# Kernel tuning notes

Measured on AMD Instinct MI355X. Metric: run time of the kernel, lower is better.

## Reference

```python
import jax, jax.numpy as jnp
import numpy as np

HEAD_SIZE = 64
N_EMBD = 768

def setup_inputs() -> dict:
    key = jax.random.key(0)
    kx, kq, kk, kv = jax.random.split(key, 4)
    x = jax.random.normal(kx, (4, 4096, N_EMBD), dtype=jnp.float32)
    s = 1.0 / np.sqrt(N_EMBD)
    Wq = jax.random.normal(kq, (N_EMBD, HEAD_SIZE), dtype=jnp.float32) * s
    Wk = jax.random.normal(kk, (N_EMBD, HEAD_SIZE), dtype=jnp.float32) * s
    Wv = jax.random.normal(kv, (N_EMBD, HEAD_SIZE), dtype=jnp.float32) * s
    return {"x": x, "Wq": Wq, "Wk": Wk, "Wv": Wv}

def reference(x, Wq, Wk, Wv):
    b, t, c = x.shape
    h = Wq.shape[1]
    q = jnp.einsum('btc,ch->bth', x, Wq)
    k = jnp.einsum('btc,ch->bth', x, Wk)
    v = jnp.einsum('btc,ch->bth', x, Wv)
    scores = jnp.einsum('bqh,bkh->bqk', q, k) / jnp.sqrt(jnp.float32(h))
    causal = jnp.tril(jnp.ones((t, t), dtype=bool))  # [t,t]
    scores = jnp.where(causal, scores, -jnp.inf)
    attn = jax.nn.softmax(scores, axis=-1)
    return jnp.einsum('bqk,bkh->bqh', attn, v)
```

## Files before the change

### kernel.cpp

```cpp
#include <hip/hip_runtime.h>
#include <math.h>

#define BB 4
#define TT 4096
#define CC 768
#define HH 64
#define NN 192
#define LDP 72
#define GR 32
#define XSTR 776
#define SC2 0.180336880f

typedef __bf16 bf16x8 __attribute__((ext_vector_type(8)));
typedef float floatx4 __attribute__((ext_vector_type(4)));
typedef float floatx16 __attribute__((ext_vector_type(16)));
typedef unsigned short u16x8 __attribute__((ext_vector_type(8)));

__device__ inline unsigned short f2bf(float f) {
    union { __bf16 b; unsigned short u; } v;
    v.b = (__bf16)f;
    return v.u;
}
__device__ inline float bf2f(unsigned short u) {
    union { unsigned int u; float f; } v;
    v.u = (unsigned int)u << 16;
    return v.f;
}
__device__ inline unsigned cvtpk(float lo, float hi) {
    unsigned d;
    asm("v_cvt_pk_bf16_f32 %0, %1, %2" : "=v"(d) : "v"(lo), "v"(hi));
    return d;
}

__global__ __launch_bounds__(256) void wprep(const float* __restrict__ Wq,
                                             const float* __restrict__ Wk,
                                             const float* __restrict__ Wv,
                                             unsigned short* __restrict__ wtf) {
    const int idx = blockIdx.x * 256 + threadIdx.x;
    if (idx >= NN * CC) return;
    const int j = idx & 7;
    const int lane = (idx >> 3) & 63;
    const int rest = idx >> 9;
    const int kg = rest % 24;
    const int n_tile = rest / 24;
    const int c = kg * 32 + (lane >> 4) * 8 + j;
    const int n = n_tile * 16 + (lane & 15);
    const float* W = (n < 64) ? Wq : (n < 128) ? Wk : Wv;
    wtf[idx] = f2bf(W[c * HH + (n & 63)]);
}

__global__ __launch_bounds__(256) void qkv_gemm(const float* __restrict__ x,
                                                const unsigned short* __restrict__ wtf,
                                                unsigned short* __restrict__ qb,
                                                unsigned short* __restrict__ kb,
                                                unsigned short* __restrict__ vbt) {
    __shared__ unsigned short As[GR * XSTR];

    const int tid = threadIdx.x;
    const int w = tid >> 6, lane = tid & 63;
    const int l15 = lane & 15, quad = lane >> 4;
    const int m0 = blockIdx.x * GR;
    const int n0 = w * 48;
    const int nt0 = w * 3;

    const float* xbase = x + (size_t)m0 * CC;
#pragma unroll
    for (int e = 0; e < 12; ++e) {
        const int c = tid + 256 * e;
        const int r = c / 96, off = (c - r * 96) * 8;
        const float4 v0 = *(const float4*)(xbase + (size_t)c * 8);
        const float4 v1 = *(const float4*)(xbase + (size_t)c * 8 + 4);
        u16x8 pk;
        pk[0] = f2bf(v0.x); pk[1] = f2bf(v0.y); pk[2] = f2bf(v0.z); pk[3] = f2bf(v0.w);
        pk[4] = f2bf(v1.x); pk[5] = f2bf(v1.y); pk[6] = f2bf(v1.z); pk[7] = f2bf(v1.w);
        *(u16x8*)(As + r * XSTR + off) = pk;
    }
    __syncthreads();

    floatx4 acc[2][3] = {};
#pragma unroll 4
    for (int step = 0; step < 12; ++step) {
        bf16x8 a0[2], a1[2];
#pragma unroll
        for (int rg = 0; rg < 2; ++rg) {
            const unsigned short* ap = As + (16 * rg + l15) * XSTR + step * 64 + quad * 8;
            a0[rg] = *(const bf16x8*)(ap);
            a1[rg] = *(const bf16x8*)(ap + 32);
        }
#pragma unroll
        for (int j = 0; j < 3; ++j) {
            const unsigned short* bp =
                wtf + ((size_t)((nt0 + j) * 24 + 2 * step) * 64 + lane) * 8;
            const bf16x8 b0 = *(const bf16x8*)(bp);
            const bf16x8 b1 = *(const bf16x8*)(bp + 512);
#pragma unroll
            for (int rg = 0; rg < 2; ++rg) {
                acc[rg][j] = __builtin_amdgcn_mfma_f32_16x16x32_bf16(a0[rg], b0, acc[rg][j], 0, 0, 0);
                acc[rg][j] = __builtin_amdgcn_mfma_f32_16x16x32_bf16(a1[rg], b1, acc[rg][j], 0, 0, 0);
            }
        }
    }

    const int b = m0 >> 12;
#pragma unroll
    for (int j = 0; j < 3; ++j) {
        const int n = n0 + j * 16 + l15;
        const int mid = n >> 6;
        const int h = n & 63;
#pragma unroll
        for (int rg = 0; rg < 2; ++rg) {
            const int tloc = (m0 & (TT - 1)) + 16 * rg + quad * 4;
            if (mid == 2) {
                ushort4 pk;
                pk.x = f2bf(acc[rg][j][0]); pk.y = f2bf(acc[rg][j][1]);
                pk.z = f2bf(acc[rg][j][2]); pk.w = f2bf(acc[rg][j][3]);
                *(ushort4*)(vbt + ((size_t)b * HH + h) * TT + tloc) = pk;
            } else {
                unsigned short* dst = (mid == 0) ? qb : kb;
#pragma unroll
                for (int r = 0; r < 4; ++r)
                    dst[(size_t)(m0 + 16 * rg + quad * 4 + r) * HH + h] = f2bf(acc[rg][j][r]);
            }
        }
    }
}

template<int CH>
__global__ __launch_bounds__(256) void attn_part(const unsigned short* __restrict__ qb,
                                                 const unsigned short* __restrict__ kb,
                                                 const unsigned short* __restrict__ vbt,
                                                 unsigned short* __restrict__ Opart,
                                                 float* __restrict__ lsum,
                                                 float* __restrict__ out) {
    __shared__ float Osh[2][2][16][64];
    __shared__ float Lsh[2][64];

    constexpr int NG = 64 / CH;
    constexpr int TOTB = CH * (NG * (NG + 1)) / 2;

    const int b = blockIdx.x & 3;
    int rem = TOTB - 1 - (blockIdx.x >> 2);
    int g = 0;
    while (rem >= CH * (g + 1)) { rem -= CH * (g + 1); ++g; }
    const int qt = g * CH + rem / (g + 1);
    const int ch = rem - (rem / (g + 1)) * (g + 1);

    const int q0  = qt * 64;
    const int tid = threadIdx.x;
    const int w = tid >> 6, lane = tid & 63;
    const int wq = w >> 1, wk = w & 1;
    const int l31 = lane & 31, hi = lane >> 5;

    const unsigned short* Qb  = qb  + (size_t)b * TT * HH;
    const unsigned short* Kb  = kb  + (size_t)b * TT * HH;
    const unsigned short* VTb = vbt + (size_t)b * HH * TT;

    bf16x8 qf[4];
    {
        const unsigned short* qp = Qb + (size_t)(q0 + 32 * wq + l31) * HH + 8 * hi;
#pragma unroll
        for (int s = 0; s < 4; ++s) qf[s] = *(const bf16x8*)(qp + 16 * s);
    }

    floatx16 o0 = {}, o1 = {};
    float lacc = 0.f;

    const int kt0 = ch * CH;
    const int kt1 = min(kt0 + CH, qt + 1);

    const unsigned short* kbase = Kb + (size_t)(32 * wk + l31) * HH + 8 * hi;
    bf16x8 kn[4];
#pragma unroll
    for (int s = 0; s < 4; ++s)
        kn[s] = *(const bf16x8*)(kbase + (size_t)kt0 * 64 * HH + 16 * s);

    for (int kt = kt0; kt < kt1; ++kt) {
        bf16x8 kc[4];
#pragma unroll
        for (int s = 0; s < 4; ++s) kc[s] = kn[s];

        bf16x8 vv[4];
#pragma unroll
        for (int i = 0; i < 4; ++i) {
            const int db = i >> 1, m = i & 1;
            vv[i] = *(const bf16x8*)(VTb + (size_t)(32 * db + l31) * TT
                                     + kt * 64 + 32 * wk + 16 * m + 8 * hi);
        }
        if (kt + 1 < kt1) {
#pragma unroll
            for (int s = 0; s < 4; ++s)
                kn[s] = *(const bf16x8*)(kbase + (size_t)(kt + 1) * 64 * HH + 16 * s);
        }

        floatx16 sa = {};
#pragma unroll
        for (int s = 0; s < 4; ++s)
            sa = __builtin_amdgcn_mfma_f32_32x32x16_bf16(kc[s], qf[s], sa, 0, 0, 0);

        float st[16];
#pragma unroll
        for (int r = 0; r < 16; ++r) st[r] = sa[r] * SC2;

        if (kt == qt) {
            const int qloc = 32 * wq + l31;
#pragma unroll
            for (int r = 0; r < 16; ++r) {
                const int kloc = 32 * wk + (r & 3) + 8 * (r >> 2) + 4 * hi;
                if (kloc > qloc) st[r] = -INFINITY;
            }
        }

#pragma unroll
        for (int r = 0; r < 16; ++r) {
            const float p = exp2f(st[r]);
            st[r] = p;
            lacc += p;
        }

        bf16x8 pf[2];
#pragma unroll
        for (int m = 0; m < 2; ++m) {
            const unsigned d0 = cvtpk(st[8 * m + 0], st[8 * m + 1]);
            const unsigned d1 = cvtpk(st[8 * m + 2], st[8 * m + 3]);
            const unsigned d2 = cvtpk(st[8 * m + 4], st[8 * m + 5]);
            const unsigned d3 = cvtpk(st[8 * m + 6], st[8 * m + 7]);
            const unsigned e0 = (unsigned)__shfl_xor((int)d0, 32);
            const unsigned e1 = (unsigned)__shfl_xor((int)d1, 32);
            const unsigned e2 = (unsigned)__shfl_xor((int)d2, 32);
            const unsigned e3 = (unsigned)__shfl_xor((int)d3, 32);
            union { unsigned u[4]; bf16x8 v; } pk;
            pk.u[0] = hi ? e2 : d0;
            pk.u[1] = hi ? e3 : d1;
            pk.u[2] = hi ? d2 : e0;
            pk.u[3] = hi ? d3 : e1;
            pf[m] = pk.v;
        }

        o0 = __builtin_amdgcn_mfma_f32_32x32x16_bf16(vv[0], pf[0], o0, 0, 0, 0);
        o0 = __builtin_amdgcn_mfma_f32_32x32x16_bf16(vv[1], pf[1], o0, 0, 0, 0);
        o1 = __builtin_amdgcn_mfma_f32_32x32x16_bf16(vv[2], pf[0], o1, 0, 0, 0);
        o1 = __builtin_amdgcn_mfma_f32_32x32x16_bf16(vv[3], pf[1], o1, 0, 0, 0);
    }

    if (wk == 1) {
#pragma unroll
        for (int r = 0; r < 16; ++r) {
            Osh[wq][0][r][lane] = o0[r];
            Osh[wq][1][r][lane] = o1[r];
        }
        Lsh[wq][lane] = lacc;
    }
    __syncthreads();
    if (wk == 1) return;
#pragma unroll
    for (int r = 0; r < 16; ++r) {
        o0[r] += Osh[wq][0][r][lane];
        o1[r] += Osh[wq][1][r][lane];
    }
    lacc += Lsh[wq][lane];
    const float l = lacc + __shfl_xor(lacc, 32);

    if (qt < CH) {
        float* outp = out + ((size_t)b * TT + q0 + 32 * wq + l31) * HH;
        const float inv = 1.f / l;
#pragma unroll
        for (int r = 0; r < 16; ++r) {
            const int dd = (r & 3) + 8 * (r >> 2) + 4 * hi;
            outp[dd]      = o0[r] * inv;
            outp[32 + dd] = o1[r] * inv;
        }
        return;
    }

    const int pbase = ((b * 64 + qt) * NG + ch) * 64;
    unsigned short* Op = Opart + ((size_t)pbase + 32 * wq + l31) * HH;
#pragma unroll
    for (int a = 0; a < 4; ++a) {
        *(unsigned*)(Op + 8 * a + 4 * hi)          = cvtpk(o0[4 * a + 0], o0[4 * a + 1]);
        *(unsigned*)(Op + 8 * a + 4 * hi + 2)      = cvtpk(o0[4 * a + 2], o0[4 * a + 3]);
        *(unsigned*)(Op + 32 + 8 * a + 4 * hi)     = cvtpk(o1[4 * a + 0], o1[4 * a + 1]);
        *(unsigned*)(Op + 32 + 8 * a + 4 * hi + 2) = cvtpk(o1[4 * a + 2], o1[4 * a + 3]);
    }
    if (hi == 0) lsum[pbase + 32 * wq + l31] = l;
}

template<int CH>
__global__ __launch_bounds__(256) void attn_merge(const unsigned short* __restrict__ Opart,
                                                  const float* __restrict__ lsum,
                                                  float* __restrict__ out) {
    constexpr int NG = 64 / CH;
    const int g = blockIdx.x * 256 + threadIdx.x;
    const int row = g >> 3, oct = g & 7;
    const int b = row >> 12, t = row & (TT - 1);
    const int qt = t >> 6, rloc = t & 63;
    if (qt < CH) return;
    const int nchunk = qt / CH + 1;
    const int pbase = ((b * 64 + qt) * NG) * 64 + rloc;
    const int d0 = oct * 8;

    float L = 0.f;
    float a[8] = {};
    for (int c = 0; c < nchunk; ++c) {
        const int idx = pbase + c * 64;
        L += lsum[idx];
        const u16x8 pv = *(const u16x8*)(Opart + (size_t)idx * HH + d0);
#pragma unroll
        for (int k = 0; k < 8; ++k) a[k] += bf2f(pv[k]);
    }
    const float inv = 1.f / L;
    float4 o0, o1;
    o0.x = a[0] * inv; o0.y = a[1] * inv; o0.z = a[2] * inv; o0.w = a[3] * inv;
    o1.x = a[4] * inv; o1.y = a[5] * inv; o1.z = a[6] * inv; o1.w = a[7] * inv;
    float* dst = out + (size_t)row * HH + d0;
    *(float4*)(dst) = o0;
    *(float4*)(dst + 4) = o1;
}

__global__ __launch_bounds__(256) void attn_full(const unsigned short* __restrict__ qb,
                                                 const unsigned short* __restrict__ kb,
                                                 const unsigned short* __restrict__ vbt,
                                                 float* __restrict__ out) {
    __shared__ unsigned short Ks[64 * LDP];
    __shared__ unsigned short VTs[64 * LDP];
    __shared__ unsigned short Ps[4][16 * LDP];

    const int b   = blockIdx.x >> 6;
    const int qt  = blockIdx.x & 63;
    const int q0  = qt * 64;
    const int tid = threadIdx.x;
    const int w = tid >> 6, lane = tid & 63;
    const int l15 = lane & 15, quad = lane >> 4;

    const unsigned short* Qb  = qb  + (size_t)b * TT * HH;
    const unsigned short* Kb  = kb  + (size_t)b * TT * HH;
    const unsigned short* VTb = vbt + (size_t)b * HH * TT;

    const int qrow = q0 + 16 * w + l15;
    const bf16x8 qf0 = *(const bf16x8*)(Qb + (size_t)qrow * HH + quad * 8);
    const bf16x8 qf1 = *(const bf16x8*)(Qb + (size_t)qrow * HH + 32 + quad * 8);

    floatx4 O[4] = {};
    floatx4 lacc = {0.f, 0.f, 0.f, 0.f};

    for (int kt = 0; kt <= qt; ++kt) {
        __syncthreads();
        const unsigned short* Kt = Kb + (size_t)(kt * 64) * HH;
        const unsigned short* Vt = VTb + kt * 64;
#pragma unroll
        for (int e = 0; e < 2; ++e) {
            const int chunk = tid + 256 * e;
            const int r = chunk >> 3, c0 = (chunk & 7) * 8;
            *(u16x8*)(Ks + r * LDP + c0)  = *(const u16x8*)(Kt + r * HH + c0);
            *(u16x8*)(VTs + r * LDP + c0) = *(const u16x8*)(Vt + (size_t)r * TT + c0);
        }
        __syncthreads();

        floatx4 s[4];
#pragma unroll
        for (int ki = 0; ki < 4; ++ki) {
            const bf16x8 kf0 = *(const bf16x8*)(Ks + (16 * ki + l15) * LDP + quad * 8);
            const bf16x8 kf1 = *(const bf16x8*)(Ks + (16 * ki + l15) * LDP + 32 + quad * 8);
            floatx4 c = {};
            c = __builtin_amdgcn_mfma_f32_16x16x32_bf16(qf0, kf0, c, 0, 0, 0);
            c = __builtin_amdgcn_mfma_f32_16x16x32_bf16(qf1, kf1, c, 0, 0, 0);
            s[ki] = c * SC2;
        }
        if (kt == qt) {
#pragma unroll
            for (int ki = 0; ki < 4; ++ki)
#pragma unroll
                for (int r = 0; r < 4; ++r)
                    if (16 * ki + l15 > 16 * w + quad * 4 + r) s[ki][r] = -INFINITY;
        }
#pragma unroll
        for (int ki = 0; ki < 4; ++ki)
#pragma unroll
            for (int r = 0; r < 4; ++r) {
                const float p = exp2f(s[ki][r]);
                s[ki][r] = p; lacc[r] += p;
            }

        unsigned short* Pw = Ps[w];
#pragma unroll
        for (int ki = 0; ki < 4; ++ki)
#pragma unroll
            for (int r = 0; r < 4; ++r)
                Pw[(quad * 4 + r) * LDP + 16 * ki + l15] = f2bf(s[ki][r]);

        const bf16x8 pf0 = *(const bf16x8*)(Pw + l15 * LDP + quad * 8);
        const bf16x8 pf1 = *(const bf16x8*)(Pw + l15 * LDP + 32 + quad * 8);
#pragma unroll
        for (int di = 0; di < 4; ++di) {
            const bf16x8 vf0 = *(const bf16x8*)(VTs + (16 * di + l15) * LDP + quad * 8);
            const bf16x8 vf1 = *(const bf16x8*)(VTs + (16 * di + l15) * LDP + 32 + quad * 8);
            O[di] = __builtin_amdgcn_mfma_f32_16x16x32_bf16(pf0, vf0, O[di], 0, 0, 0);
            O[di] = __builtin_amdgcn_mfma_f32_16x16x32_bf16(pf1, vf1, O[di], 0, 0, 0);
        }
    }
    float l_r[4];
#pragma unroll
    for (int r = 0; r < 4; ++r) {
        float v = lacc[r];
#pragma unroll
        for (int msk = 8; msk >= 1; msk >>= 1) v += __shfl_xor(v, msk, 64);
        l_r[r] = v;
    }
    float* outp = out + ((size_t)b * TT + q0 + 16 * w) * HH;
#pragma unroll
    for (int di = 0; di < 4; ++di)
#pragma unroll
        for (int r = 0; r < 4; ++r)
            outp[(quad * 4 + r) * HH + 16 * di + l15] = O[di][r] / l_r[r];
}

extern "C" void kernel_launch(void* const* d_in, const int* in_sizes, int n_in,
                              void* d_out, int out_size, void* d_ws, size_t ws_size,
                              hipStream_t stream) {
    const float* x  = (const float*)d_in[0];
    const float* Wq = (const float*)d_in[1];
    const float* Wk = (const float*)d_in[2];
    const float* Wv = (const float*)d_in[3];
    float* out = (float*)d_out;

    const size_t nQKV = (size_t)BB * TT * HH;
    unsigned short* qb  = (unsigned short*)d_ws;
    unsigned short* kb  = qb + nQKV;
    unsigned short* vbt = kb + nQKV;
    unsigned short* wtf = vbt + nQKV;
    unsigned short* Opart = wtf + (size_t)NN * CC;

    const size_t prows8  = (size_t)BB * 64 * 8 * 64;
    const size_t prows16 = (size_t)BB * 64 * 4 * 64;
    float* lsum8  = (float*)(Opart + prows8 * HH);
    float* lsum16 = (float*)(Opart + prows16 * HH);
    const size_t need8  = (size_t)((char*)(lsum8  + prows8)  - (char*)d_ws);
    const size_t need16 = (size_t)((char*)(lsum16 + prows16) - (char*)d_ws);

    wprep<<<(NN * CC + 255) / 256, 256, 0, stream>>>(Wq, Wk, Wv, wtf);
    qkv_gemm<<<(BB * TT) / GR, 256, 0, stream>>>(x, wtf, qb, kb, vbt);
    if (ws_size >= need8) {
        attn_part<8><<<BB * 288, 256, 0, stream>>>(qb, kb, vbt, Opart, lsum8, out);
        attn_merge<8><<<(BB * TT * 8) / 256, 256, 0, stream>>>(Opart, lsum8, out);
    } else if (ws_size >= need16) {
        attn_part<16><<<BB * 160, 256, 0, stream>>>(qb, kb, vbt, Opart, lsum16, out);
        attn_merge<16><<<(BB * TT * 8) / 256, 256, 0, stream>>>(Opart, lsum16, out);
    } else {
        attn_full<<<BB * (TT / 64), 256, 0, stream>>>(qb, kb, vbt, out);
    }
}
```

Measured before the change: 144.9 us.

## Stage K and V tiles through swizzled shared memory in attention kernel

Instead of each wave loading its own K and V^T fragments straight from global memory, the block now loads each 64-row K tile and V^T tile once, cooperatively, into an XOR-swizzled LDS buffer. Waves then read their MFMA operands from LDS, and the next tile is prefetched into registers. This cuts redundant global/L2 traffic, since two waves previously duplicated the K and V loads. The cost is two __syncthreads per key tile plus LDS write and read traffic, and the LDS region is reused for the final reduction buffers.

```diff
diff --git a/kernel.cpp b/kernel.cpp
--- a/kernel.cpp
+++ b/kernel.cpp
@@ -132,8 +132,11 @@
                                                  unsigned short* __restrict__ Opart,
                                                  float* __restrict__ lsum,
                                                  float* __restrict__ out) {
-    __shared__ float Osh[2][2][16][64];
-    __shared__ float Lsh[2][64];
+    __shared__ __align__(16) unsigned char smem[16896];
+    unsigned short* Ks  = (unsigned short*)smem;
+    unsigned short* VTs = (unsigned short*)(smem + 8192);
+    float (*Osh)[2][16][64] = (float(*)[2][16][64])smem;
+    float* Lsh = (float*)(smem + 16384);
 
     constexpr int NG = 64 / CH;
     constexpr int TOTB = CH * (NG * (NG + 1)) / 2;
@@ -168,28 +171,55 @@
     const int kt0 = ch * CH;
     const int kt1 = min(kt0 + CH, qt + 1);
 
-    const unsigned short* kbase = Kb + (size_t)(32 * wk + l31) * HH + 8 * hi;
-    bf16x8 kn[4];
-#pragma unroll
-    for (int s = 0; s < 4; ++s)
-        kn[s] = *(const bf16x8*)(kbase + (size_t)kt0 * 64 * HH + 16 * s);
+    const int sr = tid >> 3;
+    const int slot = tid & 7;
+    const int swz = ((slot ^ (sr & 7)) << 3);
+
+    const int kr = 32 * wk + l31;
+    const int krow_off = kr * 64;
+    const int ksw = (kr & 7);
+    const int vd0 = l31, vd1 = 32 + l31;
+
+    u16x8 nk0, nk1, nv0, nv1;
+    {
+        const unsigned short* Kt = Kb + (size_t)(kt0 * 64) * HH;
+        const unsigned short* Vt = VTb + kt0 * 64;
+        nk0 = *(const u16x8*)(Kt + (size_t)sr * HH + slot * 8);
+        nk1 = *(const u16x8*)(Kt + (size_t)(sr + 32) * HH + slot * 8);
+        nv0 = *(const u16x8*)(Vt + (size_t)sr * TT + slot * 8);
+        nv1 = *(const u16x8*)(Vt + (size_t)(sr + 32) * TT + slot * 8);
+    }
 
     for (int kt = kt0; kt < kt1; ++kt) {
+        __syncthreads();
+        *(u16x8*)(Ks  + sr * 64 + swz)        = nk0;
+        *(u16x8*)(Ks  + (sr + 32) * 64 + swz) = nk1;
+        *(u16x8*)(VTs + sr * 64 + swz)        = nv0;
+        *(u16x8*)(VTs + (sr + 32) * 64 + swz) = nv1;
+        __syncthreads();
+
+        if (kt + 1 < kt1) {
+            const unsigned short* Kt = Kb + (size_t)((kt + 1) * 64) * HH;
+            const unsigned short* Vt = VTb + (kt + 1) * 64;
+            nk0 = *(const u16x8*)(Kt + (size_t)sr * HH + slot * 8);
+            nk1 = *(const u16x8*)(Kt + (size_t)(sr + 32) * HH + slot * 8);
+            nv0 = *(const u16x8*)(Vt + (size_t)sr * TT + slot * 8);
+            nv1 = *(const u16x8*)(Vt + (size_t)(sr + 32) * TT + slot * 8);
+        }
+
         bf16x8 kc[4];
 #pragma unroll
-        for (int s = 0; s < 4; ++s) kc[s] = kn[s];
-
+        for (int s = 0; s < 4; ++s) {
+            const int sl = 2 * s + hi;
+            kc[s] = *(const bf16x8*)(Ks + krow_off + ((sl ^ ksw) << 3));
+        }
         bf16x8 vv[4];
 #pragma unroll
         for (int i = 0; i < 4; ++i) {
             const int db = i >> 1, m = i & 1;
-            vv[i] = *(const bf16x8*)(VTb + (size_t)(32 * db + l31) * TT
-                                     + kt * 64 + 32 * wk + 16 * m + 8 * hi);
-        }
-        if (kt + 1 < kt1) {
-#pragma unroll
-            for (int s = 0; s < 4; ++s)
-                kn[s] = *(const bf16x8*)(kbase + (size_t)(kt + 1) * 64 * HH + 16 * s);
+            const int d = db ? vd1 : vd0;
+            const int sl = 4 * wk + 2 * m + hi;
+            vv[i] = *(const bf16x8*)(VTs + d * 64 + ((sl ^ (d & 7)) << 3));
         }
 
         floatx16 sa = {};
@@ -242,13 +272,14 @@
         o1 = __builtin_amdgcn_mfma_f32_32x32x16_bf16(vv[3], pf[1], o1, 0, 0, 0);
     }
 
+    __syncthreads();
     if (wk == 1) {
 #pragma unroll
         for (int r = 0; r < 16; ++r) {
             Osh[wq][0][r][lane] = o0[r];
             Osh[wq][1][r][lane] = o1[r];
         }
-        Lsh[wq][lane] = lacc;
+        Lsh[wq * 64 + lane] = lacc;
     }
     __syncthreads();
     if (wk == 1) return;
@@ -257,7 +288,7 @@
         o0[r] += Osh[wq][0][r][lane];
         o1[r] += Osh[wq][1][r][lane];
     }
-    lacc += Lsh[wq][lane];
+    lacc += Lsh[wq * 64 + lane];
     const float l = lacc + __shfl_xor(lacc, 32);
 
     if (qt < CH) {
```

New measurement: 128.3 us. -11.4%, faster.
